# Kernel optimization log

Hardware: AMD Instinct MI355X
Metric: run time of the kernel (lower is better)

The kernel has to match this reference:

```python
import jax, jax.numpy as jnp
import numpy as np

NORM_EPS = 1e-6   # config.norm_eps
MAG_EPS = 1e-6    # config.magnitude_eps


def setup_inputs() -> dict:
    key = jax.random.key(0)
    k0, k1, k2, k3, k4, k5 = jax.random.split(key, 6)
    B, S, IN, OUT, R, L = 4, 2048, 2048, 2048, 4, 16
    x = jax.random.normal(k0, (B, S, IN), dtype=jnp.float32)
    # frozen quantization indices (buffer _indices), values in [0, lut_size)
    indices = jax.random.randint(k1, (OUT, IN), 0, L, dtype=jnp.int32)
    # monotonic LUT in [-1, 1] (make_lut with include_zero=False)
    lut = jnp.linspace(-1.0, 1.0, L, dtype=jnp.float32)
    scale_A = jax.random.normal(k2, (OUT, R), dtype=jnp.float32)
    scale_B = jax.random.normal(k3, (R, IN), dtype=jnp.float32)
    rank_magnitude = jax.random.uniform(k4, (R,), dtype=jnp.float32)
    bias = jax.random.normal(k5, (OUT,), dtype=jnp.float32) * 0.01
    return {"x": x, "indices": indices, "lut": lut, "scale_A": scale_A,
            "scale_B": scale_B, "rank_magnitude": rank_magnitude, "bias": bias}


def reference(x, indices, lut, scale_A, scale_B, rank_magnitude, bias):
    # _get_normalized_scales: force_positive_scales='abs', magnitude_activation='softplus'
    A = jnp.abs(scale_A)                                            # [out, r]
    A_dir = A / jnp.maximum(jnp.linalg.norm(A, axis=0, keepdims=True), NORM_EPS)
    Bm = jnp.abs(scale_B)                                           # [r, in]
    B_dir = Bm / jnp.maximum(jnp.linalg.norm(Bm, axis=1, keepdims=True), NORM_EPS)
    g = jax.nn.softplus(rank_magnitude) + MAG_EPS                   # [r]
    # LUT dequant: Q = lut[_indices], [out, in]
    Q = lut[indices]
    # rank-by-rank forward: y = sum_k g_k * (a_k \odot (Q (b_k \odot x))) + bias
    # t[b,s,r,o] = sum_i x[b,s,i] * B_dir[r,i] * Q[o,i]
    t = jnp.einsum('bsi,ri,oi->bsro', x, B_dir, Q)
    y = jnp.einsum('bsro,or,r->bso', t, A_dir, g) + bias
    return y
```

## Files before the change

kernel.cpp:

```cpp
#include <hip/hip_runtime.h>

#define IN_DIM  2048
#define OUT_DIM 2048
#define MROWS   8192
#define RANK    4

typedef unsigned short ushort_t;
typedef __attribute__((ext_vector_type(8))) short  short8;
typedef __attribute__((ext_vector_type(4))) float  floatx4;

__device__ __forceinline__ unsigned short f2bf(float f) {
  union { float f; unsigned int u; } v; v.f = f;
  unsigned int r = v.u + 0x7fffu + ((v.u >> 16) & 1u);
  return (unsigned short)(r >> 16);
}

__device__ __forceinline__ void gload16(const ushort_t* g, short* l) {
  __builtin_amdgcn_global_load_lds(
      (const __attribute__((address_space(1))) void*)g,
      (__attribute__((address_space(3))) void*)l, 16, 0, 0);
}

__global__ void coef_kernel(const float* __restrict__ sA, const float* __restrict__ sB,
                            const float* __restrict__ mag, float* __restrict__ cOut) {
  __shared__ float part[8][256];
  __shared__ float tot[8];
  int t = threadIdx.x;
  float sa[4] = {0.f, 0.f, 0.f, 0.f};
  for (int o = t; o < OUT_DIM; o += 256) {
    float4 v = *(const float4*)(sA + o * 4);
    sa[0] += v.x * v.x; sa[1] += v.y * v.y; sa[2] += v.z * v.z; sa[3] += v.w * v.w;
  }
  float sb[4] = {0.f, 0.f, 0.f, 0.f};
  for (int r = 0; r < 4; ++r)
    for (int i = t; i < IN_DIM; i += 256) { float v = sB[r * IN_DIM + i]; sb[r] += v * v; }
  for (int q = 0; q < 4; ++q) { part[q][t] = sa[q]; part[4 + q][t] = sb[q]; }
  __syncthreads();
  if (t < 8) { float s = 0.f; for (int j = 0; j < 256; ++j) s += part[t][j]; tot[t] = s; }
  __syncthreads();
  if (t < 4) {
    float g  = log1pf(expf(mag[t])) + 1e-6f;
    float na = fmaxf(sqrtf(tot[t]),     1e-6f);
    float nb = fmaxf(sqrtf(tot[4 + t]), 1e-6f);
    cOut[t] = g / (na * nb);
  }
}

__global__ void prep_kernel(const float* __restrict__ x, ushort_t* __restrict__ xb,
                            const int* __restrict__ idx, const float* __restrict__ lut,
                            const float* __restrict__ sA, const float* __restrict__ sB,
                            const float* __restrict__ c, ushort_t* __restrict__ W) {
  int t = threadIdx.x;
  if (blockIdx.x < 8192) {
    size_t i = ((size_t)blockIdx.x * 256 + t) * 8;
    float4 a = *(const float4*)(x + i);
    float4 b = *(const float4*)(x + i + 4);
    uint4 o4;
    o4.x = (unsigned)f2bf(a.x) | ((unsigned)f2bf(a.y) << 16);
    o4.y = (unsigned)f2bf(a.z) | ((unsigned)f2bf(a.w) << 16);
    o4.z = (unsigned)f2bf(b.x) | ((unsigned)f2bf(b.y) << 16);
    o4.w = (unsigned)f2bf(b.z) | ((unsigned)f2bf(b.w) << 16);
    *(uint4*)(xb + i) = o4;
  } else {
    __shared__ float aA[4];
    __shared__ float lutS[16];
    int o = blockIdx.x - 8192;
    if (t < 4)  aA[t]   = fabsf(sA[o * 4 + t]) * c[t];
    if (t < 16) lutS[t] = lut[t];
    __syncthreads();
    int i = t * 8;
    const int4* ip4 = (const int4*)(idx + (size_t)o * IN_DIM + i);
    int4 i0 = ip4[0], i1 = ip4[1];
    int ii[8] = {i0.x, i0.y, i0.z, i0.w, i1.x, i1.y, i1.z, i1.w};
    unsigned short u[8];
    #pragma unroll
    for (int j = 0; j < 8; ++j) {
      float s = aA[0] * fabsf(sB[0 * IN_DIM + i + j])
              + aA[1] * fabsf(sB[1 * IN_DIM + i + j])
              + aA[2] * fabsf(sB[2 * IN_DIM + i + j])
              + aA[3] * fabsf(sB[3 * IN_DIM + i + j]);
      u[j] = f2bf(lutS[ii[j]] * s);
    }
    uint4 o4;
    o4.x = (unsigned)u[0] | ((unsigned)u[1] << 16);
    o4.y = (unsigned)u[2] | ((unsigned)u[3] << 16);
    o4.z = (unsigned)u[4] | ((unsigned)u[5] << 16);
    o4.w = (unsigned)u[6] | ((unsigned)u[7] << 16);
    *(uint4*)(W + (size_t)o * IN_DIM + i) = o4;
  }
}

__global__ __launch_bounds__(256) void gemm_kernel(const ushort_t* __restrict__ A,
                                                   const ushort_t* __restrict__ W,
                                                   const float* __restrict__ bias,
                                                   float* __restrict__ C) {
  __shared__ short As[128 * 32];
  __shared__ short Bs[128 * 32];
  const int t    = threadIdx.x;
  const int lane = t & 63;
  const int wid  = t >> 6;
  const int wr   = wid >> 1;
  const int wc   = wid & 1;
  const int rowBase = blockIdx.y * 128;
  const int colBase = blockIdx.x * 128;

  floatx4 acc[4][4];
  #pragma unroll
  for (int i = 0; i < 4; ++i)
    #pragma unroll
    for (int j = 0; j < 4; ++j) acc[i][j] = (floatx4){0.f, 0.f, 0.f, 0.f};

  const int row0 = t >> 2;
  const int c0   = t & 3;
  const int kc0  = c0 ^ ((row0 >> 1) & 3);
  const ushort_t* a0 = A + (size_t)(rowBase + row0) * IN_DIM + kc0 * 8;
  const ushort_t* a1 = A + (size_t)(rowBase + row0 + 64) * IN_DIM + kc0 * 8;
  const ushort_t* b0 = W + (size_t)(colBase + row0) * IN_DIM + kc0 * 8;
  const ushort_t* b1 = W + (size_t)(colBase + row0 + 64) * IN_DIM + kc0 * 8;
  short* lA0 = As + (wid * 64) * 8;
  short* lA1 = As + (256 + wid * 64) * 8;
  short* lB0 = Bs + (wid * 64) * 8;
  short* lB1 = Bs + (256 + wid * 64) * 8;

  const int rA   = lane & 15;
  const int slot = ((rA >> 1) & 3) ^ (lane >> 4);
  const int kOff = slot * 8;

  for (int k0 = 0; k0 < IN_DIM; k0 += 32) {
    gload16(a0 + k0, lA0);
    gload16(a1 + k0, lA1);
    gload16(b0 + k0, lB0);
    gload16(b1 + k0, lB1);
    __syncthreads();

    short8 af[4], bf[4];
    #pragma unroll
    for (int mi = 0; mi < 4; ++mi)
      af[mi] = *(const short8*)(As + (wr * 64 + mi * 16 + rA) * 32 + kOff);
    #pragma unroll
    for (int ni = 0; ni < 4; ++ni)
      bf[ni] = *(const short8*)(Bs + (wc * 64 + ni * 16 + rA) * 32 + kOff);
    #pragma unroll
    for (int mi = 0; mi < 4; ++mi)
      #pragma unroll
      for (int ni = 0; ni < 4; ++ni)
        acc[mi][ni] = __builtin_amdgcn_mfma_f32_16x16x32_bf16(af[mi], bf[ni], acc[mi][ni], 0, 0, 0);
    __syncthreads();
  }

  const int mB = rowBase + wr * 64 + (lane >> 4) * 4;
  const int nB = colBase + wc * 64 + (lane & 15);
  #pragma unroll
  for (int ni = 0; ni < 4; ++ni) {
    float bv = bias[nB + ni * 16];
    #pragma unroll
    for (int mi = 0; mi < 4; ++mi)
      #pragma unroll
      for (int r = 0; r < 4; ++r)
        C[(size_t)(mB + mi * 16 + r) * OUT_DIM + (nB + ni * 16)] = acc[mi][ni][r] + bv;
  }
}

extern "C" void kernel_launch(void* const* d_in, const int* in_sizes, int n_in,
                              void* d_out, int out_size, void* d_ws, size_t ws_size,
                              hipStream_t stream) {
  const float* x    = (const float*)d_in[0];
  const int*   idx  = (const int*)d_in[1];
  const float* lut  = (const float*)d_in[2];
  const float* sA   = (const float*)d_in[3];
  const float* sB   = (const float*)d_in[4];
  const float* mag  = (const float*)d_in[5];
  const float* bias = (const float*)d_in[6];
  float* y = (float*)d_out;

  char* ws = (char*)d_ws;
  float*    c  = (float*)ws;
  ushort_t* W  = (ushort_t*)(ws + 256);
  ushort_t* xb = (ushort_t*)(ws + 256 + (size_t)OUT_DIM * IN_DIM * 2);

  coef_kernel<<<1, 256, 0, stream>>>(sA, sB, mag, c);
  prep_kernel<<<8192 + OUT_DIM, 256, 0, stream>>>(x, xb, idx, lut, sA, sB, c, W);
  dim3 g(OUT_DIM / 128, MROWS / 128);
  gemm_kernel<<<g, 256, 0, stream>>>(xb, W, bias, y);
}
```

Before: 243.1 us.

## Fold coefficient reduction into prep kernel and double GEMM K-tile

Removes the separate single-block coefficient kernel by having each weight-prep block recompute the scale norms and softplus magnitude redundantly, saving a launch and a serial dependency. The GEMM now loads a 64-wide K slice per iteration with an 8-way XOR swizzle and runs two MFMA sub-steps per barrier pair, halving the synchronisation count. Launch bounds now request four blocks per CU. The cost is redundant norm work across 2048 prep blocks (each rereads sA and sB) and double the LDS per GEMM block.

```diff
diff --git a/kernel.cpp b/kernel.cpp
--- a/kernel.cpp
+++ b/kernel.cpp
@@ -21,35 +21,10 @@
       (__attribute__((address_space(3))) void*)l, 16, 0, 0);
 }
 
-__global__ void coef_kernel(const float* __restrict__ sA, const float* __restrict__ sB,
-                            const float* __restrict__ mag, float* __restrict__ cOut) {
-  __shared__ float part[8][256];
-  __shared__ float tot[8];
-  int t = threadIdx.x;
-  float sa[4] = {0.f, 0.f, 0.f, 0.f};
-  for (int o = t; o < OUT_DIM; o += 256) {
-    float4 v = *(const float4*)(sA + o * 4);
-    sa[0] += v.x * v.x; sa[1] += v.y * v.y; sa[2] += v.z * v.z; sa[3] += v.w * v.w;
-  }
-  float sb[4] = {0.f, 0.f, 0.f, 0.f};
-  for (int r = 0; r < 4; ++r)
-    for (int i = t; i < IN_DIM; i += 256) { float v = sB[r * IN_DIM + i]; sb[r] += v * v; }
-  for (int q = 0; q < 4; ++q) { part[q][t] = sa[q]; part[4 + q][t] = sb[q]; }
-  __syncthreads();
-  if (t < 8) { float s = 0.f; for (int j = 0; j < 256; ++j) s += part[t][j]; tot[t] = s; }
-  __syncthreads();
-  if (t < 4) {
-    float g  = log1pf(expf(mag[t])) + 1e-6f;
-    float na = fmaxf(sqrtf(tot[t]),     1e-6f);
-    float nb = fmaxf(sqrtf(tot[4 + t]), 1e-6f);
-    cOut[t] = g / (na * nb);
-  }
-}
-
 __global__ void prep_kernel(const float* __restrict__ x, ushort_t* __restrict__ xb,
                             const int* __restrict__ idx, const float* __restrict__ lut,
                             const float* __restrict__ sA, const float* __restrict__ sB,
-                            const float* __restrict__ c, ushort_t* __restrict__ W) {
+                            const float* __restrict__ mag, ushort_t* __restrict__ W) {
   int t = threadIdx.x;
   if (blockIdx.x < 8192) {
     size_t i = ((size_t)blockIdx.x * 256 + t) * 8;
@@ -62,10 +37,29 @@
     o4.w = (unsigned)f2bf(b.z) | ((unsigned)f2bf(b.w) << 16);
     *(uint4*)(xb + i) = o4;
   } else {
+    __shared__ float part[8][256];
     __shared__ float aA[4];
     __shared__ float lutS[16];
     int o = blockIdx.x - 8192;
-    if (t < 4)  aA[t]   = fabsf(sA[o * 4 + t]) * c[t];
+    float sa[4] = {0.f, 0.f, 0.f, 0.f};
+    for (int oo = t; oo < OUT_DIM; oo += 256) {
+      float4 v = *(const float4*)(sA + oo * 4);
+      sa[0] += v.x * v.x; sa[1] += v.y * v.y; sa[2] += v.z * v.z; sa[3] += v.w * v.w;
+    }
+    float sb[4] = {0.f, 0.f, 0.f, 0.f};
+    for (int r = 0; r < 4; ++r)
+      for (int i = t; i < IN_DIM; i += 256) { float v = sB[r * IN_DIM + i]; sb[r] += v * v; }
+    #pragma unroll
+    for (int q = 0; q < 4; ++q) { part[q][t] = sa[q]; part[4 + q][t] = sb[q]; }
+    __syncthreads();
+    if (t < 8) { float s = 0.f; for (int j = 0; j < 256; ++j) s += part[t][j]; part[t][0] = s; }
+    __syncthreads();
+    if (t < 4) {
+      float g  = log1pf(expf(mag[t])) + 1e-6f;
+      float na = fmaxf(sqrtf(part[t][0]),     1e-6f);
+      float nb = fmaxf(sqrtf(part[4 + t][0]), 1e-6f);
+      aA[t] = (g / (na * nb)) * fabsf(sA[o * 4 + t]);
+    }
     if (t < 16) lutS[t] = lut[t];
     __syncthreads();
     int i = t * 8;
@@ -90,12 +84,12 @@
   }
 }
 
-__global__ __launch_bounds__(256) void gemm_kernel(const ushort_t* __restrict__ A,
-                                                   const ushort_t* __restrict__ W,
-                                                   const float* __restrict__ bias,
-                                                   float* __restrict__ C) {
-  __shared__ short As[128 * 32];
-  __shared__ short Bs[128 * 32];
+__global__ __launch_bounds__(256, 4) void gemm_kernel(const ushort_t* __restrict__ A,
+                                                      const ushort_t* __restrict__ W,
+                                                      const float* __restrict__ bias,
+                                                      float* __restrict__ C) {
+  __shared__ short As[128 * 64];
+  __shared__ short Bs[128 * 64];
   const int t    = threadIdx.x;
   const int lane = t & 63;
   const int wid  = t >> 6;
@@ -110,41 +104,44 @@
     #pragma unroll
     for (int j = 0; j < 4; ++j) acc[i][j] = (floatx4){0.f, 0.f, 0.f, 0.f};
 
-  const int row0 = t >> 2;
-  const int c0   = t & 3;
-  const int kc0  = c0 ^ ((row0 >> 1) & 3);
-  const ushort_t* a0 = A + (size_t)(rowBase + row0) * IN_DIM + kc0 * 8;
-  const ushort_t* a1 = A + (size_t)(rowBase + row0 + 64) * IN_DIM + kc0 * 8;
-  const ushort_t* b0 = W + (size_t)(colBase + row0) * IN_DIM + kc0 * 8;
-  const ushort_t* b1 = W + (size_t)(colBase + row0 + 64) * IN_DIM + kc0 * 8;
-  short* lA0 = As + (wid * 64) * 8;
-  short* lA1 = As + (256 + wid * 64) * 8;
-  short* lB0 = Bs + (wid * 64) * 8;
-  short* lB1 = Bs + (256 + wid * 64) * 8;
+  const ushort_t* ag[4]; const ushort_t* bg[4];
+  short* al[4]; short* bl[4];
+  #pragma unroll
+  for (int q = 0; q < 4; ++q) {
+    int j   = t + q * 256;
+    int row = j >> 3;
+    int kc  = (j & 7) ^ (row & 7);
+    ag[q] = A + (size_t)(rowBase + row) * IN_DIM + kc * 8;
+    bg[q] = W + (size_t)(colBase + row) * IN_DIM + kc * 8;
+    al[q] = As + ((size_t)q * 256 + wid * 64) * 8;
+    bl[q] = Bs + ((size_t)q * 256 + wid * 64) * 8;
+  }
 
-  const int rA   = lane & 15;
-  const int slot = ((rA >> 1) & 3) ^ (lane >> 4);
-  const int kOff = slot * 8;
+  const int rA = lane & 15;
+  const int kq = lane >> 4;
 
-  for (int k0 = 0; k0 < IN_DIM; k0 += 32) {
-    gload16(a0 + k0, lA0);
-    gload16(a1 + k0, lA1);
-    gload16(b0 + k0, lB0);
-    gload16(b1 + k0, lB1);
+  for (int k0 = 0; k0 < IN_DIM; k0 += 64) {
+    #pragma unroll
+    for (int q = 0; q < 4; ++q) { gload16(ag[q] + k0, al[q]); gload16(bg[q] + k0, bl[q]); }
     __syncthreads();
 
-    short8 af[4], bf[4];
     #pragma unroll
-    for (int mi = 0; mi < 4; ++mi)
-      af[mi] = *(const short8*)(As + (wr * 64 + mi * 16 + rA) * 32 + kOff);
-    #pragma unroll
-    for (int ni = 0; ni < 4; ++ni)
-      bf[ni] = *(const short8*)(Bs + (wc * 64 + ni * 16 + rA) * 32 + kOff);
-    #pragma unroll
-    for (int mi = 0; mi < 4; ++mi)
+    for (int h = 0; h < 2; ++h) {
+      const int slot = (h * 4 + kq) ^ (rA & 7);
+      const int kOff = slot * 8;
+      short8 af[4], bf[4];
+      #pragma unroll
+      for (int mi = 0; mi < 4; ++mi)
+        af[mi] = *(const short8*)(As + (wr * 64 + mi * 16 + rA) * 64 + kOff);
       #pragma unroll
       for (int ni = 0; ni < 4; ++ni)
-        acc[mi][ni] = __builtin_amdgcn_mfma_f32_16x16x32_bf16(af[mi], bf[ni], acc[mi][ni], 0, 0, 0);
+        bf[ni] = *(const short8*)(Bs + (wc * 64 + ni * 16 + rA) * 64 + kOff);
+      #pragma unroll
+      for (int mi = 0; mi < 4; ++mi)
+        #pragma unroll
+        for (int ni = 0; ni < 4; ++ni)
+          acc[mi][ni] = __builtin_amdgcn_mfma_f32_16x16x32_bf16(af[mi], bf[ni], acc[mi][ni], 0, 0, 0);
+    }
     __syncthreads();
   }
 
@@ -174,12 +171,10 @@
   float* y = (float*)d_out;
 
   char* ws = (char*)d_ws;
-  float*    c  = (float*)ws;
-  ushort_t* W  = (ushort_t*)(ws + 256);
-  ushort_t* xb = (ushort_t*)(ws + 256 + (size_t)OUT_DIM * IN_DIM * 2);
+  ushort_t* W  = (ushort_t*)ws;
+  ushort_t* xb = (ushort_t*)(ws + (size_t)OUT_DIM * IN_DIM * 2);
 
-  coef_kernel<<<1, 256, 0, stream>>>(sA, sB, mag, c);
-  prep_kernel<<<8192 + OUT_DIM, 256, 0, stream>>>(x, xb, idx, lut, sA, sB, c, W);
+  prep_kernel<<<8192 + OUT_DIM, 256, 0, stream>>>(x, xb, idx, lut, sA, sB, mag, W);
   dim3 g(OUT_DIM / 128, MROWS / 128);
   gemm_kernel<<<g, 256, 0, stream>>>(xb, W, bias, y);
 }
```

New measurement: 268.3 us. +10.4%, slower.

## Double-buffer GEMM LDS tiles and fold scale-norm kernel into prep

Applied to the files above, without the earlier changes.

The GEMM now uses two LDS buffers per operand, so the next K-slice is fetched while MFMAs run on the current one, which is meant to hide global-load latency behind compute. The separate single-block coefficient kernel is removed, and each weight-prep block recomputes the column and row norms itself using wave shuffles. This saves one kernel launch and its serialization point, at the cost of redundant norm reductions across 2048 blocks and doubled LDS use in the GEMM.

```diff
diff --git a/kernel.cpp b/kernel.cpp
--- a/kernel.cpp
+++ b/kernel.cpp
@@ -21,35 +21,10 @@
       (__attribute__((address_space(3))) void*)l, 16, 0, 0);
 }
 
-__global__ void coef_kernel(const float* __restrict__ sA, const float* __restrict__ sB,
-                            const float* __restrict__ mag, float* __restrict__ cOut) {
-  __shared__ float part[8][256];
-  __shared__ float tot[8];
-  int t = threadIdx.x;
-  float sa[4] = {0.f, 0.f, 0.f, 0.f};
-  for (int o = t; o < OUT_DIM; o += 256) {
-    float4 v = *(const float4*)(sA + o * 4);
-    sa[0] += v.x * v.x; sa[1] += v.y * v.y; sa[2] += v.z * v.z; sa[3] += v.w * v.w;
-  }
-  float sb[4] = {0.f, 0.f, 0.f, 0.f};
-  for (int r = 0; r < 4; ++r)
-    for (int i = t; i < IN_DIM; i += 256) { float v = sB[r * IN_DIM + i]; sb[r] += v * v; }
-  for (int q = 0; q < 4; ++q) { part[q][t] = sa[q]; part[4 + q][t] = sb[q]; }
-  __syncthreads();
-  if (t < 8) { float s = 0.f; for (int j = 0; j < 256; ++j) s += part[t][j]; tot[t] = s; }
-  __syncthreads();
-  if (t < 4) {
-    float g  = log1pf(expf(mag[t])) + 1e-6f;
-    float na = fmaxf(sqrtf(tot[t]),     1e-6f);
-    float nb = fmaxf(sqrtf(tot[4 + t]), 1e-6f);
-    cOut[t] = g / (na * nb);
-  }
-}
-
 __global__ void prep_kernel(const float* __restrict__ x, ushort_t* __restrict__ xb,
                             const int* __restrict__ idx, const float* __restrict__ lut,
                             const float* __restrict__ sA, const float* __restrict__ sB,
-                            const float* __restrict__ c, ushort_t* __restrict__ W) {
+                            const float* __restrict__ mag, ushort_t* __restrict__ W) {
   int t = threadIdx.x;
   if (blockIdx.x < 8192) {
     size_t i = ((size_t)blockIdx.x * 256 + t) * 8;
@@ -62,11 +37,35 @@
     o4.w = (unsigned)f2bf(b.z) | ((unsigned)f2bf(b.w) << 16);
     *(uint4*)(xb + i) = o4;
   } else {
+    __shared__ float red[8][4];
+    __shared__ float tot[8];
     __shared__ float aA[4];
     __shared__ float lutS[16];
     int o = blockIdx.x - 8192;
-    if (t < 4)  aA[t]   = fabsf(sA[o * 4 + t]) * c[t];
+    int lane = t & 63, wid = t >> 6;
+    float v[8] = {0.f, 0.f, 0.f, 0.f, 0.f, 0.f, 0.f, 0.f};
+    for (int oo = t; oo < OUT_DIM; oo += 256) {
+      float4 a = *(const float4*)(sA + oo * 4);
+      v[0] += a.x * a.x; v[1] += a.y * a.y; v[2] += a.z * a.z; v[3] += a.w * a.w;
+    }
+    for (int r = 0; r < 4; ++r)
+      for (int i = t; i < IN_DIM; i += 256) { float b = sB[r * IN_DIM + i]; v[4 + r] += b * b; }
+    for (int d = 1; d < 64; d <<= 1)
+      #pragma unroll
+      for (int q = 0; q < 8; ++q) v[q] += __shfl_xor(v[q], d, 64);
+    if (lane == 0)
+      #pragma unroll
+      for (int q = 0; q < 8; ++q) red[q][wid] = v[q];
+    __syncthreads();
+    if (t < 8) tot[t] = red[t][0] + red[t][1] + red[t][2] + red[t][3];
     if (t < 16) lutS[t] = lut[t];
+    __syncthreads();
+    if (t < 4) {
+      float g  = log1pf(expf(mag[t])) + 1e-6f;
+      float na = fmaxf(sqrtf(tot[t]),     1e-6f);
+      float nb = fmaxf(sqrtf(tot[4 + t]), 1e-6f);
+      aA[t] = (g / (na * nb)) * fabsf(sA[o * 4 + t]);
+    }
     __syncthreads();
     int i = t * 8;
     const int4* ip4 = (const int4*)(idx + (size_t)o * IN_DIM + i);
@@ -94,8 +93,8 @@
                                                    const ushort_t* __restrict__ W,
                                                    const float* __restrict__ bias,
                                                    float* __restrict__ C) {
-  __shared__ short As[128 * 32];
-  __shared__ short Bs[128 * 32];
+  __shared__ short As[2][128 * 32];
+  __shared__ short Bs[2][128 * 32];
   const int t    = threadIdx.x;
   const int lane = t & 63;
   const int wid  = t >> 6;
@@ -117,35 +116,50 @@
   const ushort_t* a1 = A + (size_t)(rowBase + row0 + 64) * IN_DIM + kc0 * 8;
   const ushort_t* b0 = W + (size_t)(colBase + row0) * IN_DIM + kc0 * 8;
   const ushort_t* b1 = W + (size_t)(colBase + row0 + 64) * IN_DIM + kc0 * 8;
-  short* lA0 = As + (wid * 64) * 8;
-  short* lA1 = As + (256 + wid * 64) * 8;
-  short* lB0 = Bs + (wid * 64) * 8;
-  short* lB1 = Bs + (256 + wid * 64) * 8;
+  short* lA0 = &As[0][(wid * 64) * 8];
+  short* lA1 = &As[0][(256 + wid * 64) * 8];
+  short* lB0 = &Bs[0][(wid * 64) * 8];
+  short* lB1 = &Bs[0][(256 + wid * 64) * 8];
 
   const int rA   = lane & 15;
   const int slot = ((rA >> 1) & 3) ^ (lane >> 4);
   const int kOff = slot * 8;
 
-  for (int k0 = 0; k0 < IN_DIM; k0 += 32) {
-    gload16(a0 + k0, lA0);
-    gload16(a1 + k0, lA1);
-    gload16(b0 + k0, lB0);
-    gload16(b1 + k0, lB1);
+#define STAGE(KK, BUF)                                                        \
+  do {                                                                        \
+    gload16(a0 + (KK), lA0 + (BUF) * 4096);                                   \
+    gload16(a1 + (KK), lA1 + (BUF) * 4096);                                   \
+    gload16(b0 + (KK), lB0 + (BUF) * 4096);                                   \
+    gload16(b1 + (KK), lB1 + (BUF) * 4096);                                   \
+  } while (0)
+
+#define COMPUTE(BUF)                                                          \
+  do {                                                                        \
+    const short* Ab = &As[BUF][0];                                            \
+    const short* Bb = &Bs[BUF][0];                                            \
+    short8 af[4], bf[4];                                                      \
+    _Pragma("unroll")                                                         \
+    for (int mi = 0; mi < 4; ++mi)                                            \
+      af[mi] = *(const short8*)(Ab + (wr * 64 + mi * 16 + rA) * 32 + kOff);   \
+    _Pragma("unroll")                                                         \
+    for (int ni = 0; ni < 4; ++ni)                                            \
+      bf[ni] = *(const short8*)(Bb + (wc * 64 + ni * 16 + rA) * 32 + kOff);   \
+    _Pragma("unroll")                                                         \
+    for (int mi = 0; mi < 4; ++mi)                                            \
+      _Pragma("unroll")                                                       \
+      for (int ni = 0; ni < 4; ++ni)                                          \
+        acc[mi][ni] = __builtin_amdgcn_mfma_f32_16x16x32_bf16(                \
+            af[mi], bf[ni], acc[mi][ni], 0, 0, 0);                            \
+  } while (0)
+
+  STAGE(0, 0);
+  for (int k0 = 0; k0 < IN_DIM; k0 += 64) {
     __syncthreads();
-
-    short8 af[4], bf[4];
-    #pragma unroll
-    for (int mi = 0; mi < 4; ++mi)
-      af[mi] = *(const short8*)(As + (wr * 64 + mi * 16 + rA) * 32 + kOff);
-    #pragma unroll
-    for (int ni = 0; ni < 4; ++ni)
-      bf[ni] = *(const short8*)(Bs + (wc * 64 + ni * 16 + rA) * 32 + kOff);
-    #pragma unroll
-    for (int mi = 0; mi < 4; ++mi)
-      #pragma unroll
-      for (int ni = 0; ni < 4; ++ni)
-        acc[mi][ni] = __builtin_amdgcn_mfma_f32_16x16x32_bf16(af[mi], bf[ni], acc[mi][ni], 0, 0, 0);
+    STAGE(k0 + 32, 1);
+    COMPUTE(0);
     __syncthreads();
+    if (k0 + 64 < IN_DIM) STAGE(k0 + 64, 0);
+    COMPUTE(1);
   }
 
   const int mB = rowBase + wr * 64 + (lane >> 4) * 4;
@@ -159,6 +173,8 @@
       for (int r = 0; r < 4; ++r)
         C[(size_t)(mB + mi * 16 + r) * OUT_DIM + (nB + ni * 16)] = acc[mi][ni][r] + bv;
   }
+#undef STAGE
+#undef COMPUTE
 }
 
 extern "C" void kernel_launch(void* const* d_in, const int* in_sizes, int n_in,
@@ -174,12 +190,10 @@
   float* y = (float*)d_out;
 
   char* ws = (char*)d_ws;
-  float*    c  = (float*)ws;
-  ushort_t* W  = (ushort_t*)(ws + 256);
-  ushort_t* xb = (ushort_t*)(ws + 256 + (size_t)OUT_DIM * IN_DIM * 2);
+  ushort_t* W  = (ushort_t*)ws;
+  ushort_t* xb = (ushort_t*)(ws + (size_t)OUT_DIM * IN_DIM * 2);
 
-  coef_kernel<<<1, 256, 0, stream>>>(sA, sB, mag, c);
-  prep_kernel<<<8192 + OUT_DIM, 256, 0, stream>>>(x, xb, idx, lut, sA, sB, c, W);
+  prep_kernel<<<8192 + OUT_DIM, 256, 0, stream>>>(x, xb, idx, lut, sA, sB, mag, W);
   dim3 g(OUT_DIM / 128, MROWS / 128);
   gemm_kernel<<<g, 256, 0, stream>>>(xb, W, bias, y);
 }
```

New measurement: 252.3 us. 3.8% more time.
